# Performance work log

Hardware: AMD Instinct MI355X
Metric: run time of the kernel (lower is better)

## Reference

```python
import jax, jax.numpy as jnp
import numpy as np

N_NODES = 100000
N_EDGES = 500000
D_IN = 128
D_HID = 256
D_OUT = 1


def mish(x):
    # x * tanh(softplus(x))
    return x * jnp.tanh(jax.nn.softplus(x))


def setup_inputs() -> dict:
    key = jax.random.key(0)
    k1, k2, k3, k4, k5, k6 = jax.random.split(key, 6)
    z = jax.random.normal(k1, (N_NODES, D_IN), dtype=jnp.float32)
    edge = jax.random.randint(k2, (2, N_EDGES), 0, N_NODES, dtype=jnp.int64)
    # PyTorch Linear default init: U(-1/sqrt(fan_in), 1/sqrt(fan_in))
    s1 = 1.0 / np.sqrt(D_IN)
    s2 = 1.0 / np.sqrt(D_HID)
    W1 = jax.random.uniform(k3, (D_HID, D_IN), minval=-s1, maxval=s1, dtype=jnp.float32)
    b1 = jax.random.uniform(k4, (D_HID,), minval=-s1, maxval=s1, dtype=jnp.float32)
    W2 = jax.random.uniform(k5, (D_OUT, D_HID), minval=-s2, maxval=s2, dtype=jnp.float32)
    b2 = jax.random.uniform(k6, (D_OUT,), minval=-s2, maxval=s2, dtype=jnp.float32)
    return {"z": z, "edge": edge, "W1": W1, "b1": b1, "W2": W2, "b2": b2}


def reference(z, edge, W1, b1, W2, b2):
    # gather node pairs and elementwise product: [E, D_IN]
    x = z[edge[0]] * z[edge[1]]
    # fc1 + mish (dropout is identity in eval mode)
    h = mish(jnp.einsum('ed,hd->eh', x, W1) + b1)
    # fc2 + sigmoid -> [E, 1]
    logits = jnp.einsum('eh,oh->eo', h, W2) + b2
    return jax.nn.sigmoid(logits)
```

## Files before the change

kernel.cpp:

```cpp
#include <hip/hip_runtime.h>
#include <hip/hip_bf16.h>
#include <hip/hip_fp16.h>
#include <type_traits>


#define N_NODES 100000
#define N_EDGES 500000
#define D_IN    128
#define D_HID   256
#define PAIRS   (N_EDGES / 32)
#define GRID    512
#define NWAVES  8
#define TOTAL_WAVES (GRID * NWAVES)
#define LDS_ROW 288

typedef _Float16 half8  __attribute__((ext_vector_type(8)));
typedef __fp16   fp16x2 __attribute__((ext_vector_type(2)));
typedef __bf16   bf16x8 __attribute__((ext_vector_type(8)));
typedef float    f32x4  __attribute__((ext_vector_type(4)));

__device__ __forceinline__ unsigned int pkh_u32(float a, float b) {
    fp16x2 r = __builtin_amdgcn_cvt_pkrtz(a, b);
    return __builtin_bit_cast(unsigned int, r);
}
__device__ __forceinline__ unsigned int pkbf_u32(float a, float b) {
    union { __hip_bfloat162 v; unsigned int u; } c;
    c.v = __float22bfloat162_rn(make_float2(a, b));
    return c.u;
}

__device__ __forceinline__ float mishf(float x) {
    float E   = __expf(fminf(x, 20.0f));
    float num = E * (E + 2.0f);
    return x * num * __builtin_amdgcn_rcpf(num + 2.0f);
}
__device__ __forceinline__ float sigf(float x) {
    return __builtin_amdgcn_rcpf(1.0f + __expf(-x));
}

__global__ __launch_bounds__(256)
void zcvt_kernel(const float* __restrict__ z, _Float16* __restrict__ zh) {
    const size_t i = (size_t)blockIdx.x * 256 + threadIdx.x;
    const float4 f0 = *reinterpret_cast<const float4*>(z + i * 8);
    const float4 f1 = *reinterpret_cast<const float4*>(z + i * 8 + 4);
    union { half8 h; uint4 u; } o;
    o.h[0] = (_Float16)f0.x; o.h[1] = (_Float16)f0.y;
    o.h[2] = (_Float16)f0.z; o.h[3] = (_Float16)f0.w;
    o.h[4] = (_Float16)f1.x; o.h[5] = (_Float16)f1.y;
    o.h[6] = (_Float16)f1.z; o.h[7] = (_Float16)f1.w;
    *reinterpret_cast<uint4*>(zh + i * 8) = o.u;
}

template <bool USE_H>
__global__ __launch_bounds__(512, 4)
void edge_mlp_kernel(const float*    __restrict__ z,
                     const _Float16* __restrict__ zh,
                     const int*      __restrict__ edge,
                     const float*    __restrict__ W1,
                     const float*    __restrict__ b1,
                     const float*    __restrict__ W2,
                     const float*    __restrict__ b2,
                     float*          __restrict__ out) {
    using frag_t = std::conditional_t<USE_H, half8, bf16x8>;

    __shared__ __align__(16) char smem[2048 + D_HID * LDS_ROW];

    const int t = threadIdx.x;

    if (t < 256) {
        ((float*)smem)[t]          = b1[t];
        ((float*)(smem + 1024))[t] = W2[t];
    }
    #pragma unroll
    for (int i = 0; i < 8; ++i) {
        const int c    = t + i * 512;
        const int h    = c >> 4;
        const int slot = c & 15;
        const float* src = W1 + h * D_IN + slot * 8;
        const float4 f0 = *reinterpret_cast<const float4*>(src);
        const float4 f1 = *reinterpret_cast<const float4*>(src + 4);
        uint4 o;
        if constexpr (USE_H) {
            o = make_uint4(pkh_u32(f0.x, f0.y), pkh_u32(f0.z, f0.w),
                           pkh_u32(f1.x, f1.y), pkh_u32(f1.z, f1.w));
        } else {
            o = make_uint4(pkbf_u32(f0.x, f0.y), pkbf_u32(f0.z, f0.w),
                           pkbf_u32(f1.x, f1.y), pkbf_u32(f1.z, f1.w));
        }
        *reinterpret_cast<uint4*>(smem + 2048 + h * LDS_ROW + slot * 16) = o;
    }
    __syncthreads();

    const int wave = t >> 6;
    const int lane = t & 63;
    const int quad = lane >> 4;
    const int nlo  = lane & 15;
    const int gw   = (blockIdx.x << 3) + wave;

    const char*  ldsA  = smem + 2048 + nlo * LDS_ROW + quad * 16;
    const float* ldsB1 = (const float*)(smem + quad * 16);
    const float* ldsW2 = (const float*)(smem + 1024 + quad * 16);
    const float  b2f   = b2[0];

    for (int pi = gw; pi < PAIRS; pi += TOTAL_WAVES) {
        const int e0 = pi * 32 + nlo;
        const int u0 = edge[e0],      v0 = edge[N_EDGES + e0];
        const int u1 = edge[e0 + 16], v1 = edge[N_EDGES + e0 + 16];

        frag_t bf0[4], bf1[4];
        if constexpr (USE_H) {
            const char* zb = reinterpret_cast<const char*>(zh) + quad * 16;
            const char* pu0 = zb + ((size_t)u0 << 8);
            const char* pv0 = zb + ((size_t)v0 << 8);
            const char* pu1 = zb + ((size_t)u1 << 8);
            const char* pv1 = zb + ((size_t)v1 << 8);
            #pragma unroll
            for (int ks = 0; ks < 4; ++ks) {
                half8 a = *reinterpret_cast<const half8*>(pu0 + ks * 64);
                half8 c = *reinterpret_cast<const half8*>(pv0 + ks * 64);
                bf0[ks] = a * c;
            }
            #pragma unroll
            for (int ks = 0; ks < 4; ++ks) {
                half8 a = *reinterpret_cast<const half8*>(pu1 + ks * 64);
                half8 c = *reinterpret_cast<const half8*>(pv1 + ks * 64);
                bf1[ks] = a * c;
            }
        } else {
            const char* zb = reinterpret_cast<const char*>(z) + quad * 32;
            const char* pu0 = zb + ((size_t)u0 << 9);
            const char* pv0 = zb + ((size_t)v0 << 9);
            const char* pu1 = zb + ((size_t)u1 << 9);
            const char* pv1 = zb + ((size_t)v1 << 9);
            #pragma unroll
            for (int ks = 0; ks < 4; ++ks) {
                float4 a0 = *reinterpret_cast<const float4*>(pu0 + ks * 128);
                float4 a1 = *reinterpret_cast<const float4*>(pu0 + ks * 128 + 16);
                float4 c0 = *reinterpret_cast<const float4*>(pv0 + ks * 128);
                float4 c1 = *reinterpret_cast<const float4*>(pv0 + ks * 128 + 16);
                union { uint4 u; bf16x8 v; } o;
                o.u = make_uint4(pkbf_u32(a0.x*c0.x, a0.y*c0.y),
                                 pkbf_u32(a0.z*c0.z, a0.w*c0.w),
                                 pkbf_u32(a1.x*c1.x, a1.y*c1.y),
                                 pkbf_u32(a1.z*c1.z, a1.w*c1.w));
                bf0[ks] = o.v;
            }
            #pragma unroll
            for (int ks = 0; ks < 4; ++ks) {
                float4 a0 = *reinterpret_cast<const float4*>(pu1 + ks * 128);
                float4 a1 = *reinterpret_cast<const float4*>(pu1 + ks * 128 + 16);
                float4 c0 = *reinterpret_cast<const float4*>(pv1 + ks * 128);
                float4 c1 = *reinterpret_cast<const float4*>(pv1 + ks * 128 + 16);
                union { uint4 u; bf16x8 v; } o;
                o.u = make_uint4(pkbf_u32(a0.x*c0.x, a0.y*c0.y),
                                 pkbf_u32(a0.z*c0.z, a0.w*c0.w),
                                 pkbf_u32(a1.x*c1.x, a1.y*c1.y),
                                 pkbf_u32(a1.z*c1.z, a1.w*c1.w));
                bf1[ks] = o.v;
            }
        }

        float l0 = 0.0f, l1 = 0.0f;
        #pragma unroll 2
        for (int g = 0; g < 16; ++g) {
            f32x4 acc0 = (f32x4){0.f, 0.f, 0.f, 0.f};
            f32x4 acc1 = (f32x4){0.f, 0.f, 0.f, 0.f};
            const char* lA = ldsA + g * (16 * LDS_ROW);
            #pragma unroll
            for (int ks = 0; ks < 4; ++ks) {
                frag_t wf = *reinterpret_cast<const frag_t*>(lA + ks * 64);
                if constexpr (USE_H) {
                    acc0 = __builtin_amdgcn_mfma_f32_16x16x32_f16(wf, bf0[ks], acc0, 0, 0, 0);
                    acc1 = __builtin_amdgcn_mfma_f32_16x16x32_f16(wf, bf1[ks], acc1, 0, 0, 0);
                } else {
                    acc0 = __builtin_amdgcn_mfma_f32_16x16x32_bf16(wf, bf0[ks], acc0, 0, 0, 0);
                    acc1 = __builtin_amdgcn_mfma_f32_16x16x32_bf16(wf, bf1[ks], acc1, 0, 0, 0);
                }
            }
            const float4 b1v = *reinterpret_cast<const float4*>(ldsB1 + g * 16);
            const float4 w2v = *reinterpret_cast<const float4*>(ldsW2 + g * 16);
            const float bb[4] = {b1v.x, b1v.y, b1v.z, b1v.w};
            const float ww[4] = {w2v.x, w2v.y, w2v.z, w2v.w};
            #pragma unroll
            for (int i = 0; i < 4; ++i) {
                l0 = fmaf(mishf(acc0[i] + bb[i]), ww[i], l0);
                l1 = fmaf(mishf(acc1[i] + bb[i]), ww[i], l1);
            }
        }

        l0 += __shfl_xor(l0, 16);  l0 += __shfl_xor(l0, 32);
        l1 += __shfl_xor(l1, 16);  l1 += __shfl_xor(l1, 32);
        if (quad == 0) {
            out[pi * 32 + nlo]      = sigf(l0 + b2f);
            out[pi * 32 + 16 + nlo] = sigf(l1 + b2f);
        }
    }
}

extern "C" void kernel_launch(void* const* d_in, const int* in_sizes, int n_in,
                              void* d_out, int out_size, void* d_ws, size_t ws_size,
                              hipStream_t stream) {
    const float* z    = (const float*)d_in[0];
    const int*   edge = (const int*)d_in[1];
    const float* W1   = (const float*)d_in[2];
    const float* b1   = (const float*)d_in[3];
    const float* W2   = (const float*)d_in[4];
    const float* b2   = (const float*)d_in[5];
    float* out = (float*)d_out;

    const size_t zh_bytes = (size_t)N_NODES * D_IN * sizeof(_Float16);
    if (d_ws != nullptr && ws_size >= zh_bytes) {
        _Float16* zh = (_Float16*)d_ws;
        zcvt_kernel<<<dim3(N_NODES * D_IN / 8 / 256), dim3(256), 0, stream>>>(z, zh);
        edge_mlp_kernel<true><<<dim3(GRID), dim3(512), 0, stream>>>(
            z, zh, edge, W1, b1, W2, b2, out);
    } else {
        edge_mlp_kernel<false><<<dim3(GRID), dim3(512), 0, stream>>>(
            z, nullptr, edge, W1, b1, W2, b2, out);
    }
}
```

Measured before the change: 163.1 us.

## Process four edge tiles per wave and fold log2e scaling into weights

Each wave now handles 64 edges per iteration instead of 32, so every W1 fragment read from LDS feeds four MFMAs instead of two. The tail iteration is handled by clamping edge indices and masking the last two stores. W1 and b1 are pre-scaled by log2(e) and W2 by ln2, so mish can use the raw v_exp_f32 (exp2) directly, and the bias is loaded into the accumulator before the MFMAs. The cost is higher register pressure from four accumulators and four fragment sets, plus extra fp16/bf16 rounding of the scaled weights.

```diff
diff --git a/kernel.cpp b/kernel.cpp
--- a/kernel.cpp
+++ b/kernel.cpp
@@ -8,12 +8,15 @@
 #define N_EDGES 500000
 #define D_IN    128
 #define D_HID   256
-#define PAIRS   (N_EDGES / 32)
+#define QUADS   ((N_EDGES + 63) / 64)
 #define GRID    512
 #define NWAVES  8
 #define TOTAL_WAVES (GRID * NWAVES)
 #define LDS_ROW 288
 
+#define LOG2E 1.44269504f
+#define LN2   0.69314718f
+
 typedef _Float16 half8  __attribute__((ext_vector_type(8)));
 typedef __fp16   fp16x2 __attribute__((ext_vector_type(2)));
 typedef __bf16   bf16x8 __attribute__((ext_vector_type(8)));
@@ -28,11 +31,8 @@
     c.v = __float22bfloat162_rn(make_float2(a, b));
     return c.u;
 }
-
-__device__ __forceinline__ float mishf(float x) {
-    float E   = __expf(fminf(x, 20.0f));
-    float num = E * (E + 2.0f);
-    return x * num * __builtin_amdgcn_rcpf(num + 2.0f);
+__device__ __forceinline__ float exp2a(float x) {
+    float r; asm("v_exp_f32 %0, %1" : "=v"(r) : "v"(x)); return r;
 }
 __device__ __forceinline__ float sigf(float x) {
     return __builtin_amdgcn_rcpf(1.0f + __expf(-x));
@@ -68,8 +68,8 @@
     const int t = threadIdx.x;
 
     if (t < 256) {
-        ((float*)smem)[t]          = b1[t];
-        ((float*)(smem + 1024))[t] = W2[t];
+        ((float*)smem)[t]          = b1[t] * LOG2E;
+        ((float*)(smem + 1024))[t] = W2[t] * LN2;
     }
     #pragma unroll
     for (int i = 0; i < 8; ++i) {
@@ -81,11 +81,15 @@
         const float4 f1 = *reinterpret_cast<const float4*>(src + 4);
         uint4 o;
         if constexpr (USE_H) {
-            o = make_uint4(pkh_u32(f0.x, f0.y), pkh_u32(f0.z, f0.w),
-                           pkh_u32(f1.x, f1.y), pkh_u32(f1.z, f1.w));
+            o = make_uint4(pkh_u32(f0.x * LOG2E, f0.y * LOG2E),
+                           pkh_u32(f0.z * LOG2E, f0.w * LOG2E),
+                           pkh_u32(f1.x * LOG2E, f1.y * LOG2E),
+                           pkh_u32(f1.z * LOG2E, f1.w * LOG2E));
         } else {
-            o = make_uint4(pkbf_u32(f0.x, f0.y), pkbf_u32(f0.z, f0.w),
-                           pkbf_u32(f1.x, f1.y), pkbf_u32(f1.z, f1.w));
+            o = make_uint4(pkbf_u32(f0.x * LOG2E, f0.y * LOG2E),
+                           pkbf_u32(f0.z * LOG2E, f0.w * LOG2E),
+                           pkbf_u32(f1.x * LOG2E, f1.y * LOG2E),
+                           pkbf_u32(f1.z * LOG2E, f1.w * LOG2E));
         }
         *reinterpret_cast<uint4*>(smem + 2048 + h * LDS_ROW + slot * 16) = o;
     }
@@ -101,70 +105,69 @@
     const float* ldsB1 = (const float*)(smem + quad * 16);
     const float* ldsW2 = (const float*)(smem + 1024 + quad * 16);
     const float  b2f   = b2[0];
-
-    for (int pi = gw; pi < PAIRS; pi += TOTAL_WAVES) {
-        const int e0 = pi * 32 + nlo;
-        const int u0 = edge[e0],      v0 = edge[N_EDGES + e0];
-        const int u1 = edge[e0 + 16], v1 = edge[N_EDGES + e0 + 16];
-
-        frag_t bf0[4], bf1[4];
+    const int    qoffH = quad * 16;
+    const int    qoffF = quad * 32;
+
+    for (int pi = gw; pi < QUADS; pi += TOTAL_WAVES) {
+        const int e0 = pi * 64 + nlo;
+        const int m1 = N_EDGES - 1;
+        const int eA = e0, eB = e0 + 16;
+        const int eC = min(e0 + 32, m1), eD = min(e0 + 48, m1);
+        const int u0 = edge[eA], v0 = edge[N_EDGES + eA];
+        const int u1 = edge[eB], v1 = edge[N_EDGES + eB];
+        const int u2 = edge[eC], v2 = edge[N_EDGES + eC];
+        const int u3 = edge[eD], v3 = edge[N_EDGES + eD];
+        const bool full = (pi != QUADS - 1);
+
+        frag_t bf0[4], bf1[4], bf2[4], bf3[4];
         if constexpr (USE_H) {
-            const char* zb = reinterpret_cast<const char*>(zh) + quad * 16;
-            const char* pu0 = zb + ((size_t)u0 << 8);
-            const char* pv0 = zb + ((size_t)v0 << 8);
-            const char* pu1 = zb + ((size_t)u1 << 8);
-            const char* pv1 = zb + ((size_t)v1 << 8);
+            const char* zb = reinterpret_cast<const char*>(zh);
+            const int ou0 = (u0 << 8) + qoffH, ov0 = (v0 << 8) + qoffH;
+            const int ou1 = (u1 << 8) + qoffH, ov1 = (v1 << 8) + qoffH;
+            const int ou2 = (u2 << 8) + qoffH, ov2 = (v2 << 8) + qoffH;
+            const int ou3 = (u3 << 8) + qoffH, ov3 = (v3 << 8) + qoffH;
             #pragma unroll
             for (int ks = 0; ks < 4; ++ks) {
-                half8 a = *reinterpret_cast<const half8*>(pu0 + ks * 64);
-                half8 c = *reinterpret_cast<const half8*>(pv0 + ks * 64);
-                bf0[ks] = a * c;
-            }
-            #pragma unroll
-            for (int ks = 0; ks < 4; ++ks) {
-                half8 a = *reinterpret_cast<const half8*>(pu1 + ks * 64);
-                half8 c = *reinterpret_cast<const half8*>(pv1 + ks * 64);
-                bf1[ks] = a * c;
+                bf0[ks] = *reinterpret_cast<const half8*>(zb + ou0 + ks * 64) *
+                          *reinterpret_cast<const half8*>(zb + ov0 + ks * 64);
+                bf1[ks] = *reinterpret_cast<const half8*>(zb + ou1 + ks * 64) *
+                          *reinterpret_cast<const half8*>(zb + ov1 + ks * 64);
+                bf2[ks] = *reinterpret_cast<const half8*>(zb + ou2 + ks * 64) *
+                          *reinterpret_cast<const half8*>(zb + ov2 + ks * 64);
+                bf3[ks] = *reinterpret_cast<const half8*>(zb + ou3 + ks * 64) *
+                          *reinterpret_cast<const half8*>(zb + ov3 + ks * 64);
             }
         } else {
-            const char* zb = reinterpret_cast<const char*>(z) + quad * 32;
-            const char* pu0 = zb + ((size_t)u0 << 9);
-            const char* pv0 = zb + ((size_t)v0 << 9);
-            const char* pu1 = zb + ((size_t)u1 << 9);
-            const char* pv1 = zb + ((size_t)v1 << 9);
-            #pragma unroll
-            for (int ks = 0; ks < 4; ++ks) {
-                float4 a0 = *reinterpret_cast<const float4*>(pu0 + ks * 128);
-                float4 a1 = *reinterpret_cast<const float4*>(pu0 + ks * 128 + 16);
-                float4 c0 = *reinterpret_cast<const float4*>(pv0 + ks * 128);
-                float4 c1 = *reinterpret_cast<const float4*>(pv0 + ks * 128 + 16);
-                union { uint4 u; bf16x8 v; } o;
-                o.u = make_uint4(pkbf_u32(a0.x*c0.x, a0.y*c0.y),
-                                 pkbf_u32(a0.z*c0.z, a0.w*c0.w),
-                                 pkbf_u32(a1.x*c1.x, a1.y*c1.y),
-                                 pkbf_u32(a1.z*c1.z, a1.w*c1.w));
-                bf0[ks] = o.v;
-            }
-            #pragma unroll
-            for (int ks = 0; ks < 4; ++ks) {
-                float4 a0 = *reinterpret_cast<const float4*>(pu1 + ks * 128);
-                float4 a1 = *reinterpret_cast<const float4*>(pu1 + ks * 128 + 16);
-                float4 c0 = *reinterpret_cast<const float4*>(pv1 + ks * 128);
-                float4 c1 = *reinterpret_cast<const float4*>(pv1 + ks * 128 + 16);
-                union { uint4 u; bf16x8 v; } o;
-                o.u = make_uint4(pkbf_u32(a0.x*c0.x, a0.y*c0.y),
-                                 pkbf_u32(a0.z*c0.z, a0.w*c0.w),
-                                 pkbf_u32(a1.x*c1.x, a1.y*c1.y),
-                                 pkbf_u32(a1.z*c1.z, a1.w*c1.w));
-                bf1[ks] = o.v;
-            }
-        }
-
-        float l0 = 0.0f, l1 = 0.0f;
+            const char* zb = reinterpret_cast<const char*>(z) + qoffF;
+            const char* pu[4] = {zb + ((size_t)u0 << 9), zb + ((size_t)u1 << 9),
+                                 zb + ((size_t)u2 << 9), zb + ((size_t)u3 << 9)};
+            const char* pv[4] = {zb + ((size_t)v0 << 9), zb + ((size_t)v1 << 9),
+                                 zb + ((size_t)v2 << 9), zb + ((size_t)v3 << 9)};
+            frag_t* bfs[4] = {bf0, bf1, bf2, bf3};
+            #pragma unroll
+            for (int tt = 0; tt < 4; ++tt) {
+                #pragma unroll
+                for (int ks = 0; ks < 4; ++ks) {
+                    float4 a0 = *reinterpret_cast<const float4*>(pu[tt] + ks * 128);
+                    float4 a1 = *reinterpret_cast<const float4*>(pu[tt] + ks * 128 + 16);
+                    float4 c0 = *reinterpret_cast<const float4*>(pv[tt] + ks * 128);
+                    float4 c1 = *reinterpret_cast<const float4*>(pv[tt] + ks * 128 + 16);
+                    union { uint4 u; bf16x8 v; } o;
+                    o.u = make_uint4(pkbf_u32(a0.x*c0.x, a0.y*c0.y),
+                                     pkbf_u32(a0.z*c0.z, a0.w*c0.w),
+                                     pkbf_u32(a1.x*c1.x, a1.y*c1.y),
+                                     pkbf_u32(a1.z*c1.z, a1.w*c1.w));
+                    bfs[tt][ks] = o.v;
+                }
+            }
+        }
+
+        float l0 = 0.0f, l1 = 0.0f, l2 = 0.0f, l3 = 0.0f;
         #pragma unroll 2
         for (int g = 0; g < 16; ++g) {
-            f32x4 acc0 = (f32x4){0.f, 0.f, 0.f, 0.f};
-            f32x4 acc1 = (f32x4){0.f, 0.f, 0.f, 0.f};
+            const float4 b1v = *reinterpret_cast<const float4*>(ldsB1 + g * 16);
+            f32x4 acc0 = (f32x4){b1v.x, b1v.y, b1v.z, b1v.w};
+            f32x4 acc1 = acc0, acc2 = acc0, acc3 = acc0;
             const char* lA = ldsA + g * (16 * LDS_ROW);
             #pragma unroll
             for (int ks = 0; ks < 4; ++ks) {
@@ -172,27 +175,58 @@
                 if constexpr (USE_H) {
                     acc0 = __builtin_amdgcn_mfma_f32_16x16x32_f16(wf, bf0[ks], acc0, 0, 0, 0);
                     acc1 = __builtin_amdgcn_mfma_f32_16x16x32_f16(wf, bf1[ks], acc1, 0, 0, 0);
+                    acc2 = __builtin_amdgcn_mfma_f32_16x16x32_f16(wf, bf2[ks], acc2, 0, 0, 0);
+                    acc3 = __builtin_amdgcn_mfma_f32_16x16x32_f16(wf, bf3[ks], acc3, 0, 0, 0);
                 } else {
                     acc0 = __builtin_amdgcn_mfma_f32_16x16x32_bf16(wf, bf0[ks], acc0, 0, 0, 0);
                     acc1 = __builtin_amdgcn_mfma_f32_16x16x32_bf16(wf, bf1[ks], acc1, 0, 0, 0);
-                }
-            }
-            const float4 b1v = *reinterpret_cast<const float4*>(ldsB1 + g * 16);
+                    acc2 = __builtin_amdgcn_mfma_f32_16x16x32_bf16(wf, bf2[ks], acc2, 0, 0, 0);
+                    acc3 = __builtin_amdgcn_mfma_f32_16x16x32_bf16(wf, bf3[ks], acc3, 0, 0, 0);
+                }
+            }
             const float4 w2v = *reinterpret_cast<const float4*>(ldsW2 + g * 16);
-            const float bb[4] = {b1v.x, b1v.y, b1v.z, b1v.w};
             const float ww[4] = {w2v.x, w2v.y, w2v.z, w2v.w};
             #pragma unroll
             for (int i = 0; i < 4; ++i) {
-                l0 = fmaf(mishf(acc0[i] + bb[i]), ww[i], l0);
-                l1 = fmaf(mishf(acc1[i] + bb[i]), ww[i], l1);
+                {
+                    float xs = acc0[i];
+                    float E  = exp2a(fminf(xs, 28.854f));
+                    float num = E * (E + 2.0f);
+                    l0 = fmaf(xs * num * __builtin_amdgcn_rcpf(num + 2.0f), ww[i], l0);
+                }
+                {
+                    float xs = acc1[i];
+                    float E  = exp2a(fminf(xs, 28.854f));
+                    float num = E * (E + 2.0f);
+                    l1 = fmaf(xs * num * __builtin_amdgcn_rcpf(num + 2.0f), ww[i], l1);
+                }
+                {
+                    float xs = acc2[i];
+                    float E  = exp2a(fminf(xs, 28.854f));
+                    float num = E * (E + 2.0f);
+                    l2 = fmaf(xs * num * __builtin_amdgcn_rcpf(num + 2.0f), ww[i], l2);
+                }
+                {
+                    float xs = acc3[i];
+                    float E  = exp2a(fminf(xs, 28.854f));
+                    float num = E * (E + 2.0f);
+                    l3 = fmaf(xs * num * __builtin_amdgcn_rcpf(num + 2.0f), ww[i], l3);
+                }
             }
         }
 
         l0 += __shfl_xor(l0, 16);  l0 += __shfl_xor(l0, 32);
         l1 += __shfl_xor(l1, 16);  l1 += __shfl_xor(l1, 32);
+        l2 += __shfl_xor(l2, 16);  l2 += __shfl_xor(l2, 32);
+        l3 += __shfl_xor(l3, 16);  l3 += __shfl_xor(l3, 32);
         if (quad == 0) {
-            out[pi * 32 + nlo]      = sigf(l0 + b2f);
-            out[pi * 32 + 16 + nlo] = sigf(l1 + b2f);
+            const int ob = pi * 64 + nlo;
+            out[ob]      = sigf(l0 + b2f);
+            out[ob + 16] = sigf(l1 + b2f);
+            if (full) {
+                out[ob + 32] = sigf(l2 + b2f);
+                out[ob + 48] = sigf(l3 + b2f);
+            }
         }
     }
 }
```

New measurement: 166.3 us. Within noise of the previous version (+1.9%).
